# Kernel tuning notes

Hardware: AMD Instinct MI355X
Metric: run time of the kernel (lower is better)

The kernel has to match this reference:

```python
import jax, jax.numpy as jnp
import numpy as np

D_MODEL = 512
N_HEADS = 8
D_HEAD = 64
INIT_RANGE = 0.02
IGNORE = -1.0e6
SINK = -1000.0


def setup_inputs() -> dict:
    key = jax.random.key(0)
    ks = jax.random.split(key, 7)
    bs, ts = 2, 128
    x = jax.random.normal(ks[0], (bs, ts, D_MODEL), dtype=jnp.float32)
    W_K1 = INIT_RANGE * jax.random.normal(ks[1], (N_HEADS, D_MODEL, D_HEAD), dtype=jnp.float32)
    W_K2 = INIT_RANGE * jax.random.normal(ks[2], (N_HEADS, D_MODEL, D_HEAD), dtype=jnp.float32)
    W_Q = INIT_RANGE * jax.random.normal(ks[3], (N_HEADS, D_MODEL, D_HEAD), dtype=jnp.float32)
    W_V12 = INIT_RANGE * jax.random.normal(ks[4], (N_HEADS, 2 * D_MODEL, D_HEAD), dtype=jnp.float32)
    W_O = INIT_RANGE * jax.random.normal(ks[5], (N_HEADS, D_HEAD, D_MODEL), dtype=jnp.float32)
    b_K1 = jnp.zeros((N_HEADS, D_HEAD), dtype=jnp.float32)
    b_K2 = jnp.zeros((N_HEADS, D_HEAD), dtype=jnp.float32)
    b_Q = jnp.zeros((N_HEADS, D_HEAD), dtype=jnp.float32)
    b_V12 = jnp.zeros((N_HEADS, D_HEAD), dtype=jnp.float32)
    b_O = jnp.zeros((D_MODEL,), dtype=jnp.float32)
    return {"x": x, "W_K1": W_K1, "W_K2": W_K2, "W_Q": W_Q, "W_V12": W_V12,
            "W_O": W_O, "b_K1": b_K1, "b_K2": b_K2, "b_Q": b_Q, "b_V12": b_V12, "b_O": b_O}


def _trittention(x, W_K1, W_K2, W_Q, W_V12, W_O, b_K1, b_K2, b_Q, b_V12, b_O):
    bs, ts, d = x.shape
    nh, dh = W_K1.shape[0], W_K1.shape[2]
    k1 = jnp.einsum('ndh,bpd->bpnh', W_K1, x) + b_K1
    k2 = jnp.einsum('ndh,bpd->bpnh', W_K2, x) + b_K2
    q = jnp.einsum('ndh,bpd->bpnh', W_Q, x) + b_Q
    # pairwise values: v[b,p,s] = cat(x[b,p], x[b,s]) @ W_V12 + b_V12
    Wa, Wb = W_V12[:, :d, :], W_V12[:, d:, :]
    va = jnp.einsum('ndh,bpd->bpnh', Wa, x)   # [b, ts, n, h]
    vb = jnp.einsum('ndh,bsd->bsnh', Wb, x)
    v = va[:, :, None] + vb[:, None] + b_V12  # [b, p, s, n, h]
    # cubic scores [b, n, s, t, q]
    scores = jnp.einsum('bsnh,btnh,bqnh->bnstq', k1, k2, q)
    ia = jnp.arange(ts)[:, None, None]  # s axis (k1)
    ib = jnp.arange(ts)[None, :, None]  # t axis (k2)
    ic = jnp.arange(ts)[None, None, :]  # q axis
    # attn_eq=False, order_attn=True
    mask = (ia >= ic) | (ib >= ic) | (ia >= ib)
    scores = jnp.where(mask, IGNORE, scores)
    # b n s t q -> b n q (s t), scale, append sink column
    scores = jnp.transpose(scores, (0, 1, 4, 2, 3)).reshape(bs, nh, ts, ts * ts) / dh
    sink = jnp.full((bs, nh, ts, 1), SINK, dtype=scores.dtype)
    attn = jax.nn.softmax(jnp.concatenate([scores, sink], axis=-1), axis=-1)
    # b p s n h -> b n h (p s), append zero value column
    vf = jnp.transpose(v, (0, 3, 4, 1, 2)).reshape(bs, nh, dh, ts * ts)
    vf = jnp.concatenate([vf, jnp.zeros((bs, nh, dh, 1), dtype=vf.dtype)], axis=-1)
    z = jnp.einsum('bnql,bnhl->bqnh', attn, vf)
    out = jnp.einsum('bpnh,nhd->bpd', z, W_O) + b_O
    return out


def reference(x, W_K1, W_K2, W_Q, W_V12, W_O, b_K1, b_K2, b_Q, b_V12, b_O):
    return _trittention(x, W_K1, W_K2, W_Q, W_V12, W_O, b_K1, b_K2, b_Q, b_V12, b_O)
```

## Files before the change

kernel.cpp:

```cpp
#include <hip/hip_runtime.h>

#define BS 2
#define TS 128
#define DM 512
#define NH 8
#define DH 64
#define BN (BS*NH)

typedef __attribute__((ext_vector_type(8))) short short8;
typedef __attribute__((ext_vector_type(4))) float floatx4;

#define SEG (BN*TS*DH)
#define OFS_Q    0
#define OFS_VA   SEG
#define OFS_VB   (2*SEG)
#define OFS_K1B  (3*SEG)
#define OFS_K2B  (3*SEG + SEG/2)
#define OFS_Z    (4*SEG)

#define N_PROJ_JOBS 160
#define N_ATTN_JOBS 1024
#define N_OUT_JOBS  1024

__device__ __forceinline__ unsigned short f2bf(float x) {
  unsigned u = __float_as_uint(x);
  u += 0x7fff + ((u >> 16) & 1);
  return (unsigned short)(u >> 16);
}
__device__ __forceinline__ float bf2f(short v) {
  return __uint_as_float(((unsigned)(unsigned short)v) << 16);
}

struct __align__(16) ProjS { short xb[64][136]; short wbt[64][136]; };
struct __align__(16) AttnS {
  short Bh[128][72]; float Rs[128]; float Cp[4][128];
  float Cs[128]; float zpart[4][64]; float dpart[4];
};
struct __align__(16) OutS  { float zt[2][520]; float zop[4][2][64]; };

__device__ __forceinline__ void proj_body(
    ProjS& u, const float* __restrict__ x,   const float* __restrict__ Wk1,
    const float* __restrict__ Wk2, const float* __restrict__ Wq,
    const float* __restrict__ Wv12,const float* __restrict__ bk1,
    const float* __restrict__ bk2, const float* __restrict__ bq,
    float* __restrict__ ws, int job, int tid, int wv, int ln, int q4, int l15)
{
  int t = job;
  int rt = t & 3; t >>= 2;
  int n  = t & 7; t >>= 3;
  int proj = t;

  const float* W;
  switch (proj) {
    case 0:  W = Wk1 + n*DM*DH;  break;
    case 1:  W = Wk2 + n*DM*DH;  break;
    case 2:  W = Wq  + n*DM*DH;  break;
    case 3:  W = Wv12 + n*2*DM*DH;  break;
    default: W = Wv12 + n*2*DM*DH + DM*DH;  break;
  }

  floatx4 acc[4];
  #pragma unroll
  for (int nt = 0; nt < 4; ++nt) acc[nt] = (floatx4){0.f,0.f,0.f,0.f};

  for (int c4k = 0; c4k < 4; ++c4k) {
    int kg0 = c4k * 128;
    #pragma unroll
    for (int p = 0; p < 8; ++p) {
      int i = p*256 + tid;
      int r = i >> 5, c = (i & 31) * 4;
      float4 xv = *(const float4*)&x[(size_t)(rt*64 + r)*DM + kg0 + c];
      uint2 pk;
      pk.x = (unsigned)f2bf(xv.x) | ((unsigned)f2bf(xv.y) << 16);
      pk.y = (unsigned)f2bf(xv.z) | ((unsigned)f2bf(xv.w) << 16);
      *(uint2*)&u.xb[r][c] = pk;
    }
    #pragma unroll
    for (int p = 0; p < 4; ++p) {
      int k0 = p*32 + wv*8;
      unsigned short tmp[8];
      #pragma unroll
      for (int jj = 0; jj < 8; ++jj)
        tmp[jj] = f2bf(W[(kg0 + k0 + jj)*DH + ln]);
      uint4 pk;
      pk.x = tmp[0] | ((unsigned)tmp[1] << 16);
      pk.y = tmp[2] | ((unsigned)tmp[3] << 16);
      pk.z = tmp[4] | ((unsigned)tmp[5] << 16);
      pk.w = tmp[6] | ((unsigned)tmp[7] << 16);
      *(uint4*)&u.wbt[ln][k0] = pk;
    }
    __syncthreads();

    short8 afr[4];
    #pragma unroll
    for (int kc = 0; kc < 4; ++kc)
      afr[kc] = *(const short8*)&u.xb[wv*16 + l15][kc*32 + q4*8];
    #pragma unroll
    for (int nt = 0; nt < 4; ++nt) {
      floatx4 c = acc[nt];
      #pragma unroll
      for (int kc = 0; kc < 4; ++kc) {
        short8 bfr = *(const short8*)&u.wbt[nt*16 + l15][kc*32 + q4*8];
        c = __builtin_amdgcn_mfma_f32_16x16x32_bf16(afr[kc], bfr, c, 0,0,0);
      }
      acc[nt] = c;
    }
    __syncthreads();
  }

  #pragma unroll
  for (int nt = 0; nt < 4; ++nt) {
    int col = nt*16 + l15;
    float bias = 0.f;
    if (proj == 0) bias = bk1[n*DH + col];
    else if (proj == 1) bias = bk2[n*DH + col];
    else if (proj == 2) bias = bq[n*DH + col];
    #pragma unroll
    for (int r = 0; r < 4; ++r) {
      int row = rt*64 + wv*16 + q4*4 + r;
      int b = row >> 7, s = row & 127;
      size_t o = (size_t)((b*NH + n)*TS + s)*DH + col;
      float v = acc[nt][r] + bias;
      switch (proj) {
        case 0: ((unsigned short*)(ws + OFS_K1B))[o] = f2bf(v); break;
        case 1: ((unsigned short*)(ws + OFS_K2B))[o] = f2bf(v); break;
        case 2: ws[OFS_Q + o] = v; break;
        case 3: ws[OFS_VA + o] = v; break;
        default: ws[OFS_VB + o] = v; break;
      }
    }
  }
}

__device__ __forceinline__ void attn_body(
    AttnS& u, const float* __restrict__ ws, const float* __restrict__ bv12,
    float* __restrict__ zb, int bn, int q, int tid, int wv, int ln,
    int q4, int l15, const short8 (&afr)[2][2])
{
  int b = bn >> 3, n = bn & 7;

  if (q < 2) {
    if (tid < 64) zb[(size_t)(b*TS + q)*DM + n*DH + tid] = 0.f;
    return;
  }

  const unsigned short* k2g = (const unsigned short*)(ws + OFS_K2B) + (size_t)bn*TS*DH;
  const float* qg  = ws + OFS_Q  + ((size_t)bn*TS + q)*DH;
  const float* vag = ws + OFS_VA + (size_t)bn*TS*DH;
  const float* vbg = ws + OFS_VB + (size_t)bn*TS*DH;

  ((float*)u.Cp)[tid] = 0.f; ((float*)u.Cp)[tid + 256] = 0.f;

  int T = (q + 15) >> 4;
  for (int i = tid; i < T*128; i += 256) {
    int r = i >> 3, c = (i & 7) * 8;
    short8 kv = *(const short8*)&k2g[r*DH + c];
    float4 q0 = *(const float4*)&qg[c];
    float4 q1 = *(const float4*)&qg[c + 4];
    unsigned short o8[8];
    o8[0] = f2bf(bf2f(kv[0]) * q0.x); o8[1] = f2bf(bf2f(kv[1]) * q0.y);
    o8[2] = f2bf(bf2f(kv[2]) * q0.z); o8[3] = f2bf(bf2f(kv[3]) * q0.w);
    o8[4] = f2bf(bf2f(kv[4]) * q1.x); o8[5] = f2bf(bf2f(kv[5]) * q1.y);
    o8[6] = f2bf(bf2f(kv[6]) * q1.z); o8[7] = f2bf(bf2f(kv[7]) * q1.w);
    uint4 pk;
    pk.x = o8[0] | ((unsigned)o8[1] << 16);
    pk.y = o8[2] | ((unsigned)o8[3] << 16);
    pk.z = o8[4] | ((unsigned)o8[5] << 16);
    pk.w = o8[6] | ((unsigned)o8[7] << 16);
    *(uint4*)&u.Bh[r][c] = pk;
  }
  __syncthreads();

  float rsum[2][4] = {{0.f,0.f,0.f,0.f},{0.f,0.f,0.f,0.f}};
  for (int tt = wv; tt < T; ++tt) {
    int tg = tt*16 + l15;
    short8 b0 = *(const short8*)&u.Bh[tg][q4*8];
    short8 b1 = *(const short8*)&u.Bh[tg][q4*8 + 32];
    float csum = 0.f;
    #pragma unroll
    for (int si2 = 0; si2 < 2; ++si2) {
      int si = wv + 4*si2;
      if (si > tt || 16*si >= q - 1) continue;
      floatx4 c = (floatx4){0.f,0.f,0.f,0.f};
      c = __builtin_amdgcn_mfma_f32_16x16x32_bf16(afr[si2][0], b0, c, 0,0,0);
      c = __builtin_amdgcn_mfma_f32_16x16x32_bf16(afr[si2][1], b1, c, 0,0,0);
      #pragma unroll
      for (int rg = 0; rg < 4; ++rg) {
        int s = si*16 + q4*4 + rg;
        float e = (s < tg && tg < q) ? __expf(c[rg] * 0.015625f) : 0.f;
        rsum[si2][rg] += e;
        csum += e;
      }
    }
    csum += __shfl_xor(csum, 16, 64);
    csum += __shfl_xor(csum, 32, 64);
    if (q4 == 0) u.Cp[wv][tg] = csum;
  }
  #pragma unroll
  for (int si2 = 0; si2 < 2; ++si2)
    #pragma unroll
    for (int rg = 0; rg < 4; ++rg) {
      float v = rsum[si2][rg];
      v += __shfl_xor(v, 1, 64); v += __shfl_xor(v, 2, 64);
      v += __shfl_xor(v, 4, 64); v += __shfl_xor(v, 8, 64);
      if (l15 == 0) u.Rs[(wv + 4*si2)*16 + q4*4 + rg] = v;
    }
  __syncthreads();

  if (tid < 128) u.Cs[tid] = u.Cp[0][tid] + u.Cp[1][tid]
                           + u.Cp[2][tid] + u.Cp[3][tid];
  __syncthreads();

  int g = wv, h = ln;
  float acc = 0.f, dp = 0.f;
  int imax = (q + 3) >> 2;
  for (int i = 0; i < imax; ++i) {
    int s = g + 4*i;
    float rv = u.Rs[s], cv = u.Cs[s];
    acc = fmaf(rv, vag[s*DH + h], acc);
    acc = fmaf(cv, vbg[s*DH + h], acc);
    dp += rv;
  }
  u.zpart[g][h] = acc;
  if (ln == 0) u.dpart[g] = dp;
  __syncthreads();

  if (tid < 64) {
    float D = u.dpart[0] + u.dpart[1] + u.dpart[2] + u.dpart[3];
    float zv = (u.zpart[0][tid] + u.zpart[1][tid]
              + u.zpart[2][tid] + u.zpart[3][tid]) / D
               + bv12[n*DH + tid];
    zb[(size_t)(b*TS + q)*DM + n*DH + tid] = zv;
  }
}

__device__ __forceinline__ void attn_pair(
    AttnS& u, const float* __restrict__ ws, const float* __restrict__ bv12,
    float* __restrict__ zb, int job, int tid, int wv, int ln, int q4, int l15)
{
  int bn = job >> 6, j = job & 63;
  const unsigned short* k1g =
      (const unsigned short*)(ws + OFS_K1B) + (size_t)bn*TS*DH;
  short8 afr[2][2];
  #pragma unroll
  for (int si2 = 0; si2 < 2; ++si2) {
    int m = (wv + 4*si2)*16 + l15;
    afr[si2][0] = *(const short8*)&k1g[m*DH + q4*8];
    afr[si2][1] = *(const short8*)&k1g[m*DH + q4*8 + 32];
  }
  attn_body(u, ws, bv12, zb, bn, j,       tid, wv, ln, q4, l15, afr);
  attn_body(u, ws, bv12, zb, bn, 127 - j, tid, wv, ln, q4, l15, afr);
}

__device__ __forceinline__ void out_job(
    OutS& u, const float* __restrict__ zb, const float* __restrict__ Wo,
    const float* __restrict__ bo, float* __restrict__ out,
    int job, int tid, int wv, int ln)
{
  int r0 = (job >> 3) * 2;
  int c0 = (job & 7) * 64;
  {
    int r = tid >> 7, c4 = (tid & 127) * 4;
    *(float4*)&u.zt[r][c4] = *(const float4*)&zb[(size_t)(r0 + r)*DM + c4];
  }
  __syncthreads();

  float a0 = 0.f, a1 = 0.f;
  const float* wp = Wo + (size_t)(wv*128)*DM + c0 + ln;
  #pragma unroll 8
  for (int kk = 0; kk < 128; ++kk) {
    float w = wp[(size_t)kk*DM];
    a0 = fmaf(u.zt[0][wv*128 + kk], w, a0);
    a1 = fmaf(u.zt[1][wv*128 + kk], w, a1);
  }
  u.zop[wv][0][ln] = a0;
  u.zop[wv][1][ln] = a1;
  __syncthreads();

  if (tid < 128) {
    int r = tid >> 6, cc = tid & 63;
    float v = u.zop[0][r][cc] + u.zop[1][r][cc]
            + u.zop[2][r][cc] + u.zop[3][r][cc] + bo[c0 + cc];
    out[(size_t)(r0 + r)*DM + c0 + cc] = v;
  }
}

__global__ __launch_bounds__(256, 4) void proj_kernel(
    const float* __restrict__ x,   const float* __restrict__ Wk1,
    const float* __restrict__ Wk2, const float* __restrict__ Wq,
    const float* __restrict__ Wv12,const float* __restrict__ bk1,
    const float* __restrict__ bk2, const float* __restrict__ bq,
    float* __restrict__ ws)
{
  __shared__ ProjS u;
  int tid = threadIdx.x;
  int wv = tid >> 6, ln = tid & 63, q4 = ln >> 4, l15 = ln & 15;
  proj_body(u, x, Wk1, Wk2, Wq, Wv12, bk1, bk2, bq, ws,
            blockIdx.x, tid, wv, ln, q4, l15);
}

__global__ __launch_bounds__(256, 4) void attn_kernel(
    const float* __restrict__ ws, const float* __restrict__ bv12,
    float* __restrict__ zb)
{
  __shared__ AttnS u;
  int tid = threadIdx.x;
  int wv = tid >> 6, ln = tid & 63, q4 = ln >> 4, l15 = ln & 15;
  attn_pair(u, ws, bv12, zb, blockIdx.x, tid, wv, ln, q4, l15);
}

__global__ __launch_bounds__(256, 4) void out_kernel(
    const float* __restrict__ zb, const float* __restrict__ Wo,
    const float* __restrict__ bo, float* __restrict__ out)
{
  __shared__ OutS u;
  int tid = threadIdx.x;
  int wv = tid >> 6, ln = tid & 63;
  out_job(u, zb, Wo, bo, out, blockIdx.x, tid, wv, ln);
}

extern "C" void kernel_launch(void* const* d_in, const int* in_sizes, int n_in,
                              void* d_out, int out_size, void* d_ws, size_t ws_size,
                              hipStream_t stream)
{
  const float* x    = (const float*)d_in[0];
  const float* Wk1  = (const float*)d_in[1];
  const float* Wk2  = (const float*)d_in[2];
  const float* Wq   = (const float*)d_in[3];
  const float* Wv12 = (const float*)d_in[4];
  const float* Wo   = (const float*)d_in[5];
  const float* bk1  = (const float*)d_in[6];
  const float* bk2  = (const float*)d_in[7];
  const float* bq   = (const float*)d_in[8];
  const float* bv12 = (const float*)d_in[9];
  const float* bo   = (const float*)d_in[10];
  float* out = (float*)d_out;
  float* ws  = (float*)d_ws;

  proj_kernel<<<N_PROJ_JOBS, 256, 0, stream>>>(x, Wk1, Wk2, Wq, Wv12,
                                               bk1, bk2, bq, ws);
  attn_kernel<<<N_ATTN_JOBS, 256, 0, stream>>>(ws, bv12, ws + OFS_Z);
  out_kernel<<<N_OUT_JOBS, 256, 0, stream>>>(ws + OFS_Z, Wo, bo, out);
}
```

Measured before the change: 112.0 us.

## Fuse attention and output projection into one kernel per query row

Merges the attention kernel and the output-projection kernel into a single kernel where each block handles one (batch, query) row. The block loops over all 8 heads, keeps the z row in shared memory and applies W_O directly, which removes the z round-trip through global memory and one launch. In exchange the grid shrinks from 1024 blocks to 256, and the causal q-dependent work is no longer balanced by j/127-j pairing. Per-block serial work across heads grows, which risks poor utilisation on the GPU.

```diff
diff --git a/kernel.cpp b/kernel.cpp
--- a/kernel.cpp
+++ b/kernel.cpp
@@ -16,11 +16,8 @@
 #define OFS_VB   (2*SEG)
 #define OFS_K1B  (3*SEG)
 #define OFS_K2B  (3*SEG + SEG/2)
-#define OFS_Z    (4*SEG)
 
 #define N_PROJ_JOBS 160
-#define N_ATTN_JOBS 1024
-#define N_OUT_JOBS  1024
 
 __device__ __forceinline__ unsigned short f2bf(float x) {
   unsigned u = __float_as_uint(x);
@@ -36,16 +33,19 @@
   short Bh[128][72]; float Rs[128]; float Cp[4][128];
   float Cs[128]; float zpart[4][64]; float dpart[4];
 };
-struct __align__(16) OutS  { float zt[2][520]; float zop[4][2][64]; };
-
-__device__ __forceinline__ void proj_body(
-    ProjS& u, const float* __restrict__ x,   const float* __restrict__ Wk1,
+
+__global__ __launch_bounds__(256, 4) void proj_kernel(
+    const float* __restrict__ x,   const float* __restrict__ Wk1,
     const float* __restrict__ Wk2, const float* __restrict__ Wq,
     const float* __restrict__ Wv12,const float* __restrict__ bk1,
     const float* __restrict__ bk2, const float* __restrict__ bq,
-    float* __restrict__ ws, int job, int tid, int wv, int ln, int q4, int l15)
+    float* __restrict__ ws)
 {
-  int t = job;
+  __shared__ ProjS u;
+  int tid = threadIdx.x;
+  int wv = tid >> 6, ln = tid & 63, q4 = ln >> 4, l15 = ln & 15;
+
+  int t = blockIdx.x;
   int rt = t & 3; t >>= 2;
   int n  = t & 7; t >>= 3;
   int proj = t;
@@ -133,21 +133,25 @@
 }
 
 __device__ __forceinline__ void attn_body(
-    AttnS& u, const float* __restrict__ ws, const float* __restrict__ bv12,
-    float* __restrict__ zb, int bn, int q, int tid, int wv, int ln,
-    int q4, int l15, const short8 (&afr)[2][2])
+    AttnS& u, float* zrow, const float* __restrict__ ws,
+    const float* __restrict__ bv12, int bn, int q, int tid, int wv, int ln,
+    int q4, int l15)
 {
-  int b = bn >> 3, n = bn & 7;
-
-  if (q < 2) {
-    if (tid < 64) zb[(size_t)(b*TS + q)*DM + n*DH + tid] = 0.f;
-    return;
-  }
-
+  int n = bn & 7;
+
+  const unsigned short* k1g = (const unsigned short*)(ws + OFS_K1B) + (size_t)bn*TS*DH;
   const unsigned short* k2g = (const unsigned short*)(ws + OFS_K2B) + (size_t)bn*TS*DH;
   const float* qg  = ws + OFS_Q  + ((size_t)bn*TS + q)*DH;
   const float* vag = ws + OFS_VA + (size_t)bn*TS*DH;
   const float* vbg = ws + OFS_VB + (size_t)bn*TS*DH;
+
+  short8 afr[2][2];
+  #pragma unroll
+  for (int si2 = 0; si2 < 2; ++si2) {
+    int m = (wv + 4*si2)*16 + l15;
+    afr[si2][0] = *(const short8*)&k1g[m*DH + q4*8];
+    afr[si2][1] = *(const short8*)&k1g[m*DH + q4*8 + 32];
+  }
 
   ((float*)u.Cp)[tid] = 0.f; ((float*)u.Cp)[tid + 256] = 0.f;
 
@@ -230,93 +234,57 @@
     float zv = (u.zpart[0][tid] + u.zpart[1][tid]
               + u.zpart[2][tid] + u.zpart[3][tid]) / D
                + bv12[n*DH + tid];
-    zb[(size_t)(b*TS + q)*DM + n*DH + tid] = zv;
-  }
-}
-
-__device__ __forceinline__ void attn_pair(
-    AttnS& u, const float* __restrict__ ws, const float* __restrict__ bv12,
-    float* __restrict__ zb, int job, int tid, int wv, int ln, int q4, int l15)
+    zrow[n*DH + tid] = zv;
+  }
+}
+
+__global__ __launch_bounds__(256, 4) void attn_out_kernel(
+    const float* __restrict__ ws, const float* __restrict__ bv12,
+    const float* __restrict__ Wo, const float* __restrict__ bo,
+    float* __restrict__ out)
 {
-  int bn = job >> 6, j = job & 63;
-  const unsigned short* k1g =
-      (const unsigned short*)(ws + OFS_K1B) + (size_t)bn*TS*DH;
-  short8 afr[2][2];
-  #pragma unroll
-  for (int si2 = 0; si2 < 2; ++si2) {
-    int m = (wv + 4*si2)*16 + l15;
-    afr[si2][0] = *(const short8*)&k1g[m*DH + q4*8];
-    afr[si2][1] = *(const short8*)&k1g[m*DH + q4*8 + 32];
-  }
-  attn_body(u, ws, bv12, zb, bn, j,       tid, wv, ln, q4, l15, afr);
-  attn_body(u, ws, bv12, zb, bn, 127 - j, tid, wv, ln, q4, l15, afr);
-}
-
-__device__ __forceinline__ void out_job(
-    OutS& u, const float* __restrict__ zb, const float* __restrict__ Wo,
-    const float* __restrict__ bo, float* __restrict__ out,
-    int job, int tid, int wv, int ln)
-{
-  int r0 = (job >> 3) * 2;
-  int c0 = (job & 7) * 64;
-  {
-    int r = tid >> 7, c4 = (tid & 127) * 4;
-    *(float4*)&u.zt[r][c4] = *(const float4*)&zb[(size_t)(r0 + r)*DM + c4];
-  }
-  __syncthreads();
-
-  float a0 = 0.f, a1 = 0.f;
-  const float* wp = Wo + (size_t)(wv*128)*DM + c0 + ln;
-  #pragma unroll 8
-  for (int kk = 0; kk < 128; ++kk) {
-    float w = wp[(size_t)kk*DM];
-    a0 = fmaf(u.zt[0][wv*128 + kk], w, a0);
-    a1 = fmaf(u.zt[1][wv*128 + kk], w, a1);
-  }
-  u.zop[wv][0][ln] = a0;
-  u.zop[wv][1][ln] = a1;
-  __syncthreads();
-
-  if (tid < 128) {
-    int r = tid >> 6, cc = tid & 63;
-    float v = u.zop[0][r][cc] + u.zop[1][r][cc]
-            + u.zop[2][r][cc] + u.zop[3][r][cc] + bo[c0 + cc];
-    out[(size_t)(r0 + r)*DM + c0 + cc] = v;
-  }
-}
-
-__global__ __launch_bounds__(256, 4) void proj_kernel(
-    const float* __restrict__ x,   const float* __restrict__ Wk1,
-    const float* __restrict__ Wk2, const float* __restrict__ Wq,
-    const float* __restrict__ Wv12,const float* __restrict__ bk1,
-    const float* __restrict__ bk2, const float* __restrict__ bq,
-    float* __restrict__ ws)
-{
-  __shared__ ProjS u;
+  __shared__ AttnS u;
+  __shared__ __align__(16) float zrow[DM];
+  __shared__ __align__(16) float zop[4][DM];
+
+  int q = blockIdx.x & 127;
+  int b = blockIdx.x >> 7;
   int tid = threadIdx.x;
   int wv = tid >> 6, ln = tid & 63, q4 = ln >> 4, l15 = ln & 15;
-  proj_body(u, x, Wk1, Wk2, Wq, Wv12, bk1, bk2, bq, ws,
-            blockIdx.x, tid, wv, ln, q4, l15);
-}
-
-__global__ __launch_bounds__(256, 4) void attn_kernel(
-    const float* __restrict__ ws, const float* __restrict__ bv12,
-    float* __restrict__ zb)
-{
-  __shared__ AttnS u;
-  int tid = threadIdx.x;
-  int wv = tid >> 6, ln = tid & 63, q4 = ln >> 4, l15 = ln & 15;
-  attn_pair(u, ws, bv12, zb, blockIdx.x, tid, wv, ln, q4, l15);
-}
-
-__global__ __launch_bounds__(256, 4) void out_kernel(
-    const float* __restrict__ zb, const float* __restrict__ Wo,
-    const float* __restrict__ bo, float* __restrict__ out)
-{
-  __shared__ OutS u;
-  int tid = threadIdx.x;
-  int wv = tid >> 6, ln = tid & 63;
-  out_job(u, zb, Wo, bo, out, blockIdx.x, tid, wv, ln);
+  float* orow = out + (size_t)(b*TS + q)*DM;
+
+  if (q < 2) {
+    orow[tid]       = bo[tid];
+    orow[tid + 256] = bo[tid + 256];
+    return;
+  }
+
+  #pragma unroll 1
+  for (int n = 0; n < NH; ++n)
+    attn_body(u, zrow, ws, bv12, b*NH + n, q, tid, wv, ln, q4, l15);
+  __syncthreads();
+
+  #pragma unroll
+  for (int p = 0; p < 2; ++p) {
+    int c = p*256 + ln*4;
+    float4 a = {0.f, 0.f, 0.f, 0.f};
+    const float* wp = Wo + (size_t)(wv*128)*DM + c;
+    #pragma unroll 8
+    for (int kk = 0; kk < 128; ++kk) {
+      float4 w = *(const float4*)(wp + (size_t)kk*DM);
+      float zk = zrow[wv*128 + kk];
+      a.x = fmaf(zk, w.x, a.x); a.y = fmaf(zk, w.y, a.y);
+      a.z = fmaf(zk, w.z, a.z); a.w = fmaf(zk, w.w, a.w);
+    }
+    *(float4*)&zop[wv][c] = a;
+  }
+  __syncthreads();
+
+  #pragma unroll
+  for (int p = 0; p < 2; ++p) {
+    int c = p*256 + tid;
+    orow[c] = zop[0][c] + zop[1][c] + zop[2][c] + zop[3][c] + bo[c];
+  }
 }
 
 extern "C" void kernel_launch(void* const* d_in, const int* in_sizes, int n_in,
@@ -339,6 +307,5 @@
 
   proj_kernel<<<N_PROJ_JOBS, 256, 0, stream>>>(x, Wk1, Wk2, Wq, Wv12,
                                                bk1, bk2, bq, ws);
-  attn_kernel<<<N_ATTN_JOBS, 256, 0, stream>>>(ws, bv12, ws + OFS_Z);
-  out_kernel<<<N_OUT_JOBS, 256, 0, stream>>>(ws + OFS_Z, Wo, bo, out);
-}
+  attn_out_kernel<<<BS*TS, 256, 0, stream>>>(ws, bv12, Wo, bo, out);
+}
```

Result: slower. 152.9 us (+36.5%).
